# Optimization experiments

Hardware: AMD Instinct MI355X
Metric: run time of the kernel (lower is better)

## Reference

```python
import jax, jax.numpy as jnp
import numpy as np
import math

HIDDEN = 2048
NUM_HEADS = 16
NUM_KV_HEADS = 4
HEAD_DIM = HIDDEN // NUM_HEADS  # 128
INTER = 8192
ROPE_THETA = 10000.0
EPS = 1e-6
B, S = 1, 2048


def _linear_init(key, out_f, in_f):
    return jax.random.normal(key, (out_f, in_f), dtype=jnp.float32) * (2.0 / (in_f + out_f)) ** 0.5


def setup_inputs() -> dict:
    key = jax.random.key(0)
    ks = jax.random.split(key, 10)
    hidden_states = jax.random.normal(ks[0], (B, S, HIDDEN), dtype=jnp.float32)
    # additive causal mask [B, 1, S, S]
    causal = jnp.tril(jnp.ones((S, S), dtype=bool))
    attention_mask = jnp.where(causal, 0.0, -1e9).astype(jnp.float32)[None, None]
    position_ids = jnp.arange(S, dtype=jnp.int32)[None, :]
    return {
        "hidden_states": hidden_states,
        "attention_mask": attention_mask,
        "position_ids": position_ids,
        "norm1_w": jnp.ones((HIDDEN,), dtype=jnp.float32),
        "norm2_w": jnp.ones((HIDDEN,), dtype=jnp.float32),
        "Wq": _linear_init(ks[1], NUM_HEADS * HEAD_DIM, HIDDEN),
        "Wk": _linear_init(ks[2], NUM_KV_HEADS * HEAD_DIM, HIDDEN),
        "Wv": _linear_init(ks[3], NUM_KV_HEADS * HEAD_DIM, HIDDEN),
        "Wo": _linear_init(ks[4], HIDDEN, NUM_HEADS * HEAD_DIM),
        "Wgate": _linear_init(ks[5], INTER, HIDDEN),
        "Wup": _linear_init(ks[6], INTER, HIDDEN),
        "Wdown": _linear_init(ks[7], HIDDEN, INTER),
    }


def _rmsnorm(x, w):
    return x * jax.lax.rsqrt(jnp.mean(x * x, axis=-1, keepdims=True) + EPS) * w


def _apply_rope(x, position_ids):
    # x: [B, H, S, D]; split-half RoPE exactly as the torch module does
    half = x.shape[-1] // 2
    inv_freq = (1.0 / (ROPE_THETA ** (jnp.arange(0, HEAD_DIM, 2, dtype=jnp.float32) / HEAD_DIM)))[:half]
    freqs = jnp.einsum('bi,j->bij', position_ids.astype(jnp.float32), inv_freq)  # [B,S,half]
    cos = jnp.cos(freqs)[:, None]  # [B,1,S,half]
    sin = jnp.sin(freqs)[:, None]
    x1, x2 = x[..., :half], x[..., half:]
    return jnp.concatenate([x1 * cos - x2 * sin, x2 * cos + x1 * sin], axis=-1)


def reference(hidden_states, attention_mask, position_ids, norm1_w, norm2_w,
              Wq, Wk, Wv, Wo, Wgate, Wup, Wdown):
    b, s, _ = hidden_states.shape
    # --- attention sub-block (pre-norm residual) ---
    h = _rmsnorm(hidden_states, norm1_w)
    q = (h @ Wq.T).reshape(b, s, NUM_HEADS, HEAD_DIM).transpose(0, 2, 1, 3)
    k = (h @ Wk.T).reshape(b, s, NUM_KV_HEADS, HEAD_DIM).transpose(0, 2, 1, 3)
    v = (h @ Wv.T).reshape(b, s, NUM_KV_HEADS, HEAD_DIM).transpose(0, 2, 1, 3)
    q = _apply_rope(q, position_ids)
    k = _apply_rope(k, position_ids)
    n_rep = NUM_HEADS // NUM_KV_HEADS
    k = jnp.repeat(k, n_rep, axis=1)  # GQA repeat_interleave over head dim
    v = jnp.repeat(v, n_rep, axis=1)
    scores = jnp.einsum('bhqd,bhkd->bhqk', q, k) / math.sqrt(HEAD_DIM)
    scores = scores + attention_mask
    attn = jax.nn.softmax(scores, axis=-1)
    ctx = jnp.einsum('bhqk,bhkd->bhqd', attn, v).transpose(0, 2, 1, 3).reshape(b, s, -1)
    x = hidden_states + ctx @ Wo.T
    # --- MoE sub-block: num_experts == 1 -> plain SwiGLU MLP ---
    h2 = _rmsnorm(x, norm2_w)
    mlp = (jax.nn.silu(h2 @ Wgate.T) * (h2 @ Wup.T)) @ Wdown.T
    return x + mlp
```

## Files before the change

kernel.cpp:

```cpp
#include <hip/hip_runtime.h>
#include <hip/hip_bf16.h>
#include <math.h>


#define HIDDENC 2048
#define SLEN    2048
#define NHEADS  16
#define NKV     4
#define HD      128
#define INTERC  8192

typedef __attribute__((ext_vector_type(8))) short bf16x8;
typedef __attribute__((ext_vector_type(4))) float f32x4;
typedef __hip_bfloat16 bf16;

__device__ __forceinline__ void gld_lds16(const void* g, void* l) {
    __builtin_amdgcn_global_load_lds((const __attribute__((address_space(1))) void*)g,
                                     (__attribute__((address_space(3))) void*)l, 16, 0, 0);
}

__device__ __forceinline__ unsigned short bf_bits(float x) {
    bf16 t = __float2bfloat16(x);
    return *(unsigned short*)&t;
}
__device__ __forceinline__ float bits_f(short s) {
    bf16 b = *(bf16*)&s;
    return __bfloat162float(b);
}

#define SBAR      asm volatile("s_barrier" ::: "memory")
#define WAIT_VM4  asm volatile("s_waitcnt vmcnt(4)" ::: "memory")
#define WAIT_VM0  asm volatile("s_waitcnt vmcnt(0)" ::: "memory")

template <int EPI>
__global__ __launch_bounds__(256) void gemm_bt(const bf16* __restrict__ A,
                                               const bf16* __restrict__ B,
                                               void* __restrict__ Cout,
                                               const float* __restrict__ R,
                                               int M, int N, int K, int lda) {
    constexpr int BM = 128, BN = 128, BK = 64;
    __shared__ bf16 As[BM * BK];
    __shared__ bf16 Bs[BN * BK];
    const int tid  = threadIdx.x;
    const int wave = tid >> 6;
    const int lane = tid & 63;
    const int wm = wave >> 1, wn = wave & 1;
    const long m0 = (long)blockIdx.y * BM;
    const long n0 = (long)blockIdx.x * BN;

    const int srow = wave * 8 + (lane >> 3);
    const int scol = (lane & 7) * 8;
    const bf16* Ag = A + (m0 + srow) * (long)lda + scol;
    const bf16* Bg = B + (n0 + srow) * (long)lda + scol;
    bf16* Asw = &As[(wave * 8) * BK];
    bf16* Bsw = &Bs[(wave * 8) * BK];

    f32x4 acc[4][4] = {};
    const int row = lane & 15;
    const int kq  = (lane >> 4) * 8;

    for (int k0 = 0; k0 < K; k0 += BK) {
#pragma unroll
        for (int t = 0; t < 4; t++) {
            gld_lds16(Ag + (long)(t * 32) * lda + k0, Asw + t * 32 * BK);
            gld_lds16(Bg + (long)(t * 32) * lda + k0, Bsw + t * 32 * BK);
        }
        __syncthreads();
#pragma unroll
        for (int kk = 0; kk < BK; kk += 32) {
            bf16x8 af[4], bfr[4];
#pragma unroll
            for (int i = 0; i < 4; i++)
                af[i] = *(const bf16x8*)&As[(wm * 64 + i * 16 + row) * BK + kk + kq];
#pragma unroll
            for (int j = 0; j < 4; j++)
                bfr[j] = *(const bf16x8*)&Bs[(wn * 64 + j * 16 + row) * BK + kk + kq];
#pragma unroll
            for (int i = 0; i < 4; i++)
#pragma unroll
                for (int j = 0; j < 4; j++)
                    acc[i][j] = __builtin_amdgcn_mfma_f32_16x16x32_bf16(af[i], bfr[j], acc[i][j], 0, 0, 0);
        }
        __syncthreads();
    }

    const int quad = lane >> 4;
#pragma unroll
    for (int i = 0; i < 4; i++)
#pragma unroll
        for (int j = 0; j < 4; j++)
#pragma unroll
            for (int r = 0; r < 4; r++) {
                long rr = m0 + wm * 64 + i * 16 + quad * 4 + r;
                long cc = n0 + wn * 64 + j * 16 + (lane & 15);
                float v = acc[i][j][r];
                if (EPI == 0) {
                    ((bf16*)Cout)[rr * N + cc] = __float2bfloat16(v);
                } else {
                    ((float*)Cout)[rr * N + cc] = v + R[rr * N + cc];
                }
            }
}

template <int EPI>
__global__ __launch_bounds__(512) void gemm256(const bf16* __restrict__ A,
                                               const bf16* __restrict__ B,
                                               void* __restrict__ Cout,
                                               int M, int N, int K, int lda) {
    __shared__ __align__(16) bf16 smem[2][2][256 * 64];
    const int tid  = threadIdx.x;
    const int wave = tid >> 6, lane = tid & 63;
    const int wm = wave >> 2, wn = wave & 3;
    const int quad = lane >> 4, lrow = lane & 15;
    const long m0 = (long)blockIdx.y * 256;
    const long n0 = (long)blockIdx.x * 256;
    const long kofs = (long)blockIdx.z * K;

    const int srow  = tid >> 3;
    const int gphys = tid & 7;
    const int glog  = gphys ^ (srow & 7);
    const bf16* Ag = A + (m0 + srow) * (long)lda + kofs + glog * 8;
    const bf16* Bg = B + (n0 + srow) * (long)lda + kofs + glog * 8;

    auto stageA = [&](int tt) {
#pragma unroll
        for (int rr = 0; rr < 4; rr++)
            gld_lds16(Ag + ((long)tt << 6) + (long)(rr * 64) * lda,
                      &smem[tt & 1][0][tid * 8 + rr * 4096]);
    };
    auto stageB = [&](int tt, int hh) {
#pragma unroll
        for (int r2 = 0; r2 < 2; r2++) {
            int rr = hh * 2 + r2;
            gld_lds16(Bg + ((long)tt << 6) + (long)(rr * 64) * lda,
                      &smem[tt & 1][1][tid * 8 + rr * 4096]);
        }
    };

    f32x4 acc[8][4] = {};
    const int swz = (quad ^ (lrow & 7)) * 8;
    const int NT = K >> 6;

    stageA(0);
    stageB(0, 0); stageB(0, 1);
    if (NT > 1) { stageB(1, 0); stageB(1, 1); }
    WAIT_VM4;
    SBAR;

    for (int t = 0; t < NT; ++t) {
        const bf16* smA = &smem[t & 1][0][0];
        const bf16* smB = &smem[t & 1][1][0];
        bf16x8 bq[4][2], aq[2][2];

#pragma unroll
        for (int n = 0; n < 4; n++)
#pragma unroll
            for (int ks = 0; ks < 2; ks++)
                bq[n][ks] = *(const bf16x8*)&smB[(wn * 64 + n * 16 + lrow) * 64 + (swz ^ (ks * 32))];
#pragma unroll
        for (int i = 0; i < 2; i++)
#pragma unroll
            for (int ks = 0; ks < 2; ks++)
                aq[i][ks] = *(const bf16x8*)&smA[(wm * 128 + i * 16 + lrow) * 64 + (swz ^ (ks * 32))];
        if (t + 1 < NT) stageA(t + 1);
        SBAR;
        __builtin_amdgcn_s_setprio(1);
#pragma unroll
        for (int i = 0; i < 2; i++)
#pragma unroll
            for (int n = 0; n < 4; n++) {
                acc[i][n] = __builtin_amdgcn_mfma_f32_16x16x32_bf16(aq[i][0], bq[n][0], acc[i][n], 0, 0, 0);
                acc[i][n] = __builtin_amdgcn_mfma_f32_16x16x32_bf16(aq[i][1], bq[n][1], acc[i][n], 0, 0, 0);
            }
        __builtin_amdgcn_s_setprio(0);
        SBAR;

#pragma unroll
        for (int q = 1; q < 4; q++) {
#pragma unroll
            for (int i = 0; i < 2; i++)
#pragma unroll
                for (int ks = 0; ks < 2; ks++)
                    aq[i][ks] = *(const bf16x8*)&smA[(wm * 128 + (q * 2 + i) * 16 + lrow) * 64 + (swz ^ (ks * 32))];
            if (q == 1) { if (t + 2 < NT) stageB(t + 2, 0); }
            if (q == 2) { if (t + 2 < NT) stageB(t + 2, 1); }
            SBAR;
            __builtin_amdgcn_s_setprio(1);
#pragma unroll
            for (int i = 0; i < 2; i++)
#pragma unroll
                for (int n = 0; n < 4; n++) {
                    acc[q * 2 + i][n] = __builtin_amdgcn_mfma_f32_16x16x32_bf16(aq[i][0], bq[n][0], acc[q * 2 + i][n], 0, 0, 0);
                    acc[q * 2 + i][n] = __builtin_amdgcn_mfma_f32_16x16x32_bf16(aq[i][1], bq[n][1], acc[q * 2 + i][n], 0, 0, 0);
                }
            __builtin_amdgcn_s_setprio(0);
            if (q == 3) {
                if (t + 2 < NT) { WAIT_VM4; } else { WAIT_VM0; }
            }
            SBAR;
        }
    }

#pragma unroll
    for (int i = 0; i < 8; i++)
#pragma unroll
        for (int n = 0; n < 4; n++)
#pragma unroll
            for (int r = 0; r < 4; r++) {
                long rr = m0 + wm * 128 + i * 16 + quad * 4 + r;
                long cc = n0 + wn * 64 + n * 16 + lrow;
                float v = acc[i][n][r];
                if (EPI == 0) {
                    ((bf16*)Cout)[rr * N + cc] = __float2bfloat16(v);
                } else {
                    ((float*)Cout)[(long)blockIdx.z * M * N + rr * N + cc] = v;
                }
            }
}

__global__ __launch_bounds__(256) void rmsnorm_kernel(const float* __restrict__ x,
                                                      const float* __restrict__ w,
                                                      bf16* __restrict__ out) {
    const int row = blockIdx.x;
    const int tid = threadIdx.x;
    const float* xr = x + (long)row * HIDDENC;
    float4 a = *(const float4*)&xr[tid * 8];
    float4 b = *(const float4*)&xr[tid * 8 + 4];
    float ss = a.x*a.x + a.y*a.y + a.z*a.z + a.w*a.w + b.x*b.x + b.y*b.y + b.z*b.z + b.w*b.w;
#pragma unroll
    for (int d = 1; d < 64; d <<= 1) ss += __shfl_xor(ss, d, 64);
    __shared__ float wsum[4];
    if ((tid & 63) == 0) wsum[tid >> 6] = ss;
    __syncthreads();
    ss = wsum[0] + wsum[1] + wsum[2] + wsum[3];
    float sc = rsqrtf(ss * (1.0f / HIDDENC) + 1e-6f);
    float4 wa = *(const float4*)&w[tid * 8];
    float4 wb = *(const float4*)&w[tid * 8 + 4];
    float vals[8] = {a.x*wa.x, a.y*wa.y, a.z*wa.z, a.w*wa.w,
                     b.x*wb.x, b.y*wb.y, b.z*wb.z, b.w*wb.w};
    union { bf16x8 v; unsigned short u[8]; } pk;
#pragma unroll
    for (int e = 0; e < 8; e++) pk.u[e] = bf_bits(vals[e] * sc);
    *(bf16x8*)&out[(long)row * HIDDENC + tid * 8] = pk.v;
}

__global__ __launch_bounds__(256) void cvt_kernel(const float* __restrict__ in,
                                                  bf16* __restrict__ out, long n) {
    long idx = ((long)blockIdx.x * 256 + threadIdx.x) * 8;
    if (idx >= n) return;
    float4 a = *(const float4*)&in[idx];
    float4 b = *(const float4*)&in[idx + 4];
    float vals[8] = {a.x, a.y, a.z, a.w, b.x, b.y, b.z, b.w};
    union { bf16x8 v; unsigned short u[8]; } pk;
#pragma unroll
    for (int e = 0; e < 8; e++) pk.u[e] = bf_bits(vals[e]);
    *(bf16x8*)&out[idx] = pk.v;
}

__global__ __launch_bounds__(256) void rope_kernel(bf16* __restrict__ x,
                                                   const int* __restrict__ pos,
                                                   int nheads, int rowstride) {
    long gid = (long)blockIdx.x * 256 + threadIdx.x;
    int i = gid & 63;
    long t = gid >> 6;
    int h = (int)(t % nheads);
    long s = t / nheads;
    if (s >= SLEN) return;
    float inv = __expf(-(float)i * 0.14391156516779195f);
    float f = (float)pos[s] * inv;
    float sn, c;
    sincosf(f, &sn, &c);
    bf16* p = x + s * (long)rowstride + h * HD + i;
    float x1 = __bfloat162float(p[0]);
    float x2 = __bfloat162float(p[64]);
    p[0]  = __float2bfloat16(x1 * c - x2 * sn);
    p[64] = __float2bfloat16(x2 * c + x1 * sn);
}

__global__ __launch_bounds__(256) void flash_attn(const bf16* __restrict__ Q,
                                                  const bf16* __restrict__ Kb,
                                                  const bf16* __restrict__ VT,
                                                  bf16* __restrict__ Ctx) {
    constexpr int QSTR = 2560, PSTR = 68, BKEY = 64;
    __shared__ bf16 Ks[64 * 128];
    __shared__ bf16 Vs[128 * 64];
    __shared__ bf16 Ps[4][16 * PSTR];
    const int qt  = 31 - blockIdx.x;
    const int h   = blockIdx.y;
    const int kvh = h >> 2;
    const int tid = threadIdx.x;
    const int wave = tid >> 6, lane = tid & 63;
    const int quad = lane >> 4, lrow = lane & 15;
    const int qbase = qt * 64 + wave * 16;

    bf16x8 qf[4];
#pragma unroll
    for (int kk = 0; kk < 4; kk++)
        qf[kk] = *(const bf16x8*)&Q[(long)(qbase + lrow) * QSTR + h * HD + kk * 32 + quad * 8];

    f32x4 o[8] = {};
    float mrow[4], lsum[4];
#pragma unroll
    for (int r = 0; r < 4; r++) { mrow[r] = -1e30f; lsum[r] = 0.0f; }

    const int nkt = qt + 1;
    const float scale = 0.08838834764831845f;
    const bf16* Kh  = Kb + kvh * HD;
    const bf16* VTh = VT + (long)(kvh * HD) * SLEN;
    bf16* Pw = Ps[wave];

    for (int kt = 0; kt < nkt; kt++) {
        __syncthreads();
#pragma unroll
        for (int rd = 0; rd < 4; rd++) {
            int id = rd * 256 + tid;
            int row = id >> 4, g = id & 15;
            bf16x8 kv = *(const bf16x8*)&Kh[(long)(kt * BKEY + row) * QSTR + g * 8];
            *(bf16x8*)&Ks[row * 128 + ((g ^ (row & 15)) * 8)] = kv;
        }
#pragma unroll
        for (int rd = 0; rd < 4; rd++) {
            int id = rd * 256 + tid;
            int d = id >> 3, g = id & 7;
            bf16x8 vv = *(const bf16x8*)&VTh[(long)d * SLEN + kt * BKEY + g * 8];
            *(bf16x8*)&Vs[d * 64 + ((g ^ (d & 7)) * 8)] = vv;
        }
        __syncthreads();

        f32x4 sacc[4] = {};
#pragma unroll
        for (int kk = 0; kk < 4; kk++) {
            bf16x8 kb[4];
#pragma unroll
            for (int j = 0; j < 4; j++)
                kb[j] = *(const bf16x8*)&Ks[(j * 16 + lrow) * 128 + (((kk * 4 + quad) ^ lrow) * 8)];
#pragma unroll
            for (int j = 0; j < 4; j++)
                sacc[j] = __builtin_amdgcn_mfma_f32_16x16x32_bf16(qf[kk], kb[j], sacc[j], 0, 0, 0);
        }

        const bool diag = (kt == qt);
#pragma unroll
        for (int j = 0; j < 4; j++)
#pragma unroll
            for (int r = 0; r < 4; r++) {
                float v = sacc[j][r] * scale;
                if (diag) {
                    int rowg = qbase + quad * 4 + r;
                    int colg = qt * 64 + j * 16 + lrow;
                    if (colg > rowg) v = -1e30f;
                }
                sacc[j][r] = v;
            }

        float alpha[4];
#pragma unroll
        for (int r = 0; r < 4; r++) {
            float mx = sacc[0][r];
#pragma unroll
            for (int j = 1; j < 4; j++) mx = fmaxf(mx, sacc[j][r]);
#pragma unroll
            for (int d = 1; d < 16; d <<= 1) mx = fmaxf(mx, __shfl_xor(mx, d, 16));
            float mnew = fmaxf(mrow[r], mx);
            float a = __expf(mrow[r] - mnew);
            mrow[r] = mnew;
            alpha[r] = a;
            float rs = 0.0f;
#pragma unroll
            for (int j = 0; j < 4; j++) {
                float p = __expf(sacc[j][r] - mnew);
                sacc[j][r] = p;
                rs += p;
            }
#pragma unroll
            for (int d = 1; d < 16; d <<= 1) rs += __shfl_xor(rs, d, 16);
            lsum[r] = lsum[r] * a + rs;
        }

#pragma unroll
        for (int dj = 0; dj < 8; dj++)
#pragma unroll
            for (int r = 0; r < 4; r++) o[dj][r] *= alpha[r];

#pragma unroll
        for (int j = 0; j < 4; j++)
#pragma unroll
            for (int r = 0; r < 4; r++)
                Pw[(quad * 4 + r) * PSTR + j * 16 + lrow] = __float2bfloat16(sacc[j][r]);
        __asm__ volatile("s_waitcnt lgkmcnt(0)" ::: "memory");

#pragma unroll
        for (int kk = 0; kk < 2; kk++) {
            bf16x8 pf = *(const bf16x8*)&Pw[lrow * PSTR + kk * 32 + quad * 8];
#pragma unroll
            for (int dj = 0; dj < 8; dj++) {
                int dr = dj * 16 + lrow;
                bf16x8 vb = *(const bf16x8*)&Vs[dr * 64 + (((kk * 4 + quad) ^ (dr & 7)) * 8)];
                o[dj] = __builtin_amdgcn_mfma_f32_16x16x32_bf16(pf, vb, o[dj], 0, 0, 0);
            }
        }
    }

#pragma unroll
    for (int dj = 0; dj < 8; dj++)
#pragma unroll
        for (int r = 0; r < 4; r++) {
            long rowg = qbase + quad * 4 + r;
            long col  = (long)h * HD + dj * 16 + lrow;
            Ctx[rowg * (NHEADS * HD) + col] = __float2bfloat16(o[dj][r] / lsum[r]);
        }
}

__global__ __launch_bounds__(256) void silu_mul_kernel(const bf16* __restrict__ g,
                                                       const bf16* __restrict__ u,
                                                       bf16* __restrict__ out, long n) {
    long idx = ((long)blockIdx.x * 256 + threadIdx.x) * 8;
    if (idx >= n) return;
    bf16x8 gv = *(const bf16x8*)&g[idx];
    bf16x8 uv = *(const bf16x8*)&u[idx];
    union { bf16x8 v; unsigned short w[8]; } pk;
#pragma unroll
    for (int e = 0; e < 8; e++) {
        float gf = bits_f(gv[e]);
        float uf = bits_f(uv[e]);
        float s = gf / (1.0f + __expf(-gf));
        pk.w[e] = bf_bits(s * uf);
    }
    *(bf16x8*)&out[idx] = pk.v;
}

__global__ __launch_bounds__(256) void reduce4_kernel(const float* __restrict__ p,
                                                      float* __restrict__ out, long n) {
    long idx = ((long)blockIdx.x * 256 + threadIdx.x) * 4;
    if (idx >= n) return;
    float4 a = *(const float4*)&p[idx];
    float4 b = *(const float4*)&p[idx + n];
    float4 c = *(const float4*)&p[idx + 2 * n];
    float4 d = *(const float4*)&p[idx + 3 * n];
    float4 o = *(const float4*)&out[idx];
    o.x += a.x + b.x + c.x + d.x;
    o.y += a.y + b.y + c.y + d.y;
    o.z += a.z + b.z + c.z + d.z;
    o.w += a.w + b.w + c.w + d.w;
    *(float4*)&out[idx] = o;
}

extern "C" void kernel_launch(void* const* d_in, const int* in_sizes, int n_in,
                              void* d_out, int out_size, void* d_ws, size_t ws_size,
                              hipStream_t stream) {
    const float* hidden = (const float*)d_in[0];
    const int*   pos    = (const int*)d_in[2];
    const float* n1w    = (const float*)d_in[3];
    const float* n2w    = (const float*)d_in[4];
    const float* Wq     = (const float*)d_in[5];
    const float* Wk     = (const float*)d_in[6];
    const float* Wv     = (const float*)d_in[7];
    const float* Wo     = (const float*)d_in[8];
    const float* Wg     = (const float*)d_in[9];
    const float* Wu     = (const float*)d_in[10];
    const float* Wd     = (const float*)d_in[11];
    float* out = (float*)d_out;

    char* ws = (char*)d_ws;
    const size_t MB = 1ull << 20;
    bf16* h    = (bf16*)(ws + 0);
    bf16* qk   = (bf16*)(ws + 8  * MB);
    bf16* vt   = (bf16*)(ws + 18 * MB);
    bf16* ctx  = (bf16*)(ws + 20 * MB);
    bf16* wqk  = (bf16*)(ws + 28 * MB);
    bf16* wvb  = (bf16*)(ws + 38 * MB);
    bf16*  wg   = (bf16*)(ws + 8   * MB);
    bf16*  wu   = (bf16*)(ws + 40  * MB);
    bf16*  gate = (bf16*)(ws + 72  * MB);
    bf16*  up   = (bf16*)(ws + 104 * MB);
    bf16*  wd   = (bf16*)(ws + 104 * MB);
    float* pbuf = (float*)(ws + 0);
    bf16* wob = wqk;

    rmsnorm_kernel<<<dim3(2048), dim3(256), 0, stream>>>(hidden, n1w, h);
    cvt_kernel<<<dim3(2048), dim3(256), 0, stream>>>(Wq, wqk,                2048L * 2048);
    cvt_kernel<<<dim3(512),  dim3(256), 0, stream>>>(Wk, wqk + 2048L * 2048, 512L * 2048);
    cvt_kernel<<<dim3(512),  dim3(256), 0, stream>>>(Wv, wvb,                512L * 2048);
    gemm_bt<0><<<dim3(20, 16), dim3(256), 0, stream>>>(h, wqk, qk, nullptr, 2048, 2560, 2048, 2048);
    gemm_bt<0><<<dim3(16, 4),  dim3(256), 0, stream>>>(wvb, h, vt, nullptr, 512, 2048, 2048, 2048);
    rope_kernel<<<dim3(8192), dim3(256), 0, stream>>>(qk, pos, NHEADS, 2560);
    rope_kernel<<<dim3(2048), dim3(256), 0, stream>>>(qk + 2048, pos, NKV, 2560);
    flash_attn<<<dim3(32, 16), dim3(256), 0, stream>>>(qk, qk + 2048, vt, ctx);
    cvt_kernel<<<dim3(2048), dim3(256), 0, stream>>>(Wo, wob, 2048L * 2048);
    gemm_bt<1><<<dim3(16, 16), dim3(256), 0, stream>>>(ctx, wob, out, hidden, 2048, 2048, 2048, 2048);
    rmsnorm_kernel<<<dim3(2048), dim3(256), 0, stream>>>(out, n2w, h);
    cvt_kernel<<<dim3(8192), dim3(256), 0, stream>>>(Wg, wg, 8192L * 2048);
    cvt_kernel<<<dim3(8192), dim3(256), 0, stream>>>(Wu, wu, 8192L * 2048);
    gemm256<0><<<dim3(32, 8), dim3(512), 0, stream>>>(h, wg, gate, 2048, 8192, 2048, 2048);
    gemm256<0><<<dim3(32, 8), dim3(512), 0, stream>>>(h, wu, up,   2048, 8192, 2048, 2048);
    silu_mul_kernel<<<dim3(8192), dim3(256), 0, stream>>>(gate, up, gate, 2048L * 8192);
    cvt_kernel<<<dim3(8192), dim3(256), 0, stream>>>(Wd, wd, 2048L * 8192);
    gemm256<2><<<dim3(8, 8, 4), dim3(512), 0, stream>>>(gate, wd, pbuf, 2048, 2048, 2048, 8192);
    reduce4_kernel<<<dim3(4096), dim3(256), 0, stream>>>(pbuf, out, 2048L * 2048);
    (void)in_sizes; (void)n_in; (void)out_size; (void)ws_size;
}
```

Before: 758.3 us.

## Split attention KV range across two blocks with async LDS double-buffering; fuse SiLU-mul into up GEMM

Flash attention now launches two blocks per query tile, each handling alternating key tiles. Each block writes fp32 partial outputs plus row max and sum, and a new combine kernel merges the two halves. K/V loads use global_load_lds into double-buffered shared memory with priority hints around the MFMA sections, aiming to hide load latency and balance the causal workload. The SiLU-multiply is folded into the up-projection GEMM epilogue, which reads gate in place and removes the separate elementwise pass and the up buffer. The cost is extra fp32 traffic for the partials and one additional kernel launch.

```diff
diff --git a/kernel.cpp b/kernel.cpp
--- a/kernel.cpp
+++ b/kernel.cpp
@@ -106,6 +106,7 @@
 __global__ __launch_bounds__(512) void gemm256(const bf16* __restrict__ A,
                                                const bf16* __restrict__ B,
                                                void* __restrict__ Cout,
+                                               const bf16* __restrict__ Gg,
                                                int M, int N, int K, int lda) {
     __shared__ __align__(16) bf16 smem[2][2][256 * 64];
     const int tid  = threadIdx.x;
@@ -212,8 +213,12 @@
                 float v = acc[i][n][r];
                 if (EPI == 0) {
                     ((bf16*)Cout)[rr * N + cc] = __float2bfloat16(v);
+                } else if (EPI == 2) {
+                    ((float*)Cout)[(long)blockIdx.z * M * N + rr * N + cc] = v;
                 } else {
-                    ((float*)Cout)[(long)blockIdx.z * M * N + rr * N + cc] = v;
+                    float g = __bfloat162float(Gg[rr * N + cc]);
+                    float sg = g / (1.0f + __expf(-g));
+                    ((bf16*)Cout)[rr * N + cc] = __float2bfloat16(sg * v);
                 }
             }
 }
@@ -280,12 +285,14 @@
 __global__ __launch_bounds__(256) void flash_attn(const bf16* __restrict__ Q,
                                                   const bf16* __restrict__ Kb,
                                                   const bf16* __restrict__ VT,
-                                                  bf16* __restrict__ Ctx) {
+                                                  float* __restrict__ Opart,
+                                                  float* __restrict__ Ml) {
     constexpr int QSTR = 2560, PSTR = 68, BKEY = 64;
-    __shared__ bf16 Ks[64 * 128];
-    __shared__ bf16 Vs[128 * 64];
+    __shared__ bf16 Ks[2][64 * 128];
+    __shared__ bf16 Vs[2][128 * 64];
     __shared__ bf16 Ps[4][16 * PSTR];
-    const int qt  = 31 - blockIdx.x;
+    const int qt  = 31 - (int)(blockIdx.x >> 1);
+    const int sp  = blockIdx.x & 1;
     const int h   = blockIdx.y;
     const int kvh = h >> 2;
     const int tid = threadIdx.x;
@@ -303,41 +310,48 @@
 #pragma unroll
     for (int r = 0; r < 4; r++) { mrow[r] = -1e30f; lsum[r] = 0.0f; }
 
-    const int nkt = qt + 1;
     const float scale = 0.08838834764831845f;
     const bf16* Kh  = Kb + kvh * HD;
     const bf16* VTh = VT + (long)(kvh * HD) * SLEN;
     bf16* Pw = Ps[wave];
 
-    for (int kt = 0; kt < nkt; kt++) {
-        __syncthreads();
-#pragma unroll
-        for (int rd = 0; rd < 4; rd++) {
-            int id = rd * 256 + tid;
-            int row = id >> 4, g = id & 15;
-            bf16x8 kv = *(const bf16x8*)&Kh[(long)(kt * BKEY + row) * QSTR + g * 8];
-            *(bf16x8*)&Ks[row * 128 + ((g ^ (row & 15)) * 8)] = kv;
-        }
-#pragma unroll
-        for (int rd = 0; rd < 4; rd++) {
-            int id = rd * 256 + tid;
-            int d = id >> 3, g = id & 7;
-            bf16x8 vv = *(const bf16x8*)&VTh[(long)d * SLEN + kt * BKEY + g * 8];
-            *(bf16x8*)&Vs[d * 64 + ((g ^ (d & 7)) * 8)] = vv;
-        }
-        __syncthreads();
+    const int glogK = (tid & 15) ^ ((tid >> 4) & 15);
+    const int glogV = (tid & 7) ^ ((tid >> 3) & 7);
+    const bf16* KgB = Kh + (long)(tid >> 4) * QSTR + glogK * 8;
+    const bf16* VgB = VTh + (long)(tid >> 3) * SLEN + glogV * 8;
+
+    auto stage = [&](int kt, int b) {
+#pragma unroll
+        for (int rd = 0; rd < 4; rd++)
+            gld_lds16(KgB + (long)(kt * BKEY + rd * 16) * QSTR,
+                      &Ks[b][(rd * 256 + tid) * 8]);
+#pragma unroll
+        for (int rd = 0; rd < 4; rd++)
+            gld_lds16(VgB + (long)(rd * 32) * SLEN + kt * BKEY,
+                      &Vs[b][(rd * 256 + tid) * 8]);
+    };
+
+    int cur = 0;
+    stage(sp, 0);
+    WAIT_VM0;
+    __syncthreads();
+
+    for (int kt = sp; kt <= qt; kt += 2) {
+        if (kt + 2 <= qt) stage(kt + 2, cur ^ 1);
 
         f32x4 sacc[4] = {};
+        __builtin_amdgcn_s_setprio(1);
 #pragma unroll
         for (int kk = 0; kk < 4; kk++) {
             bf16x8 kb[4];
 #pragma unroll
             for (int j = 0; j < 4; j++)
-                kb[j] = *(const bf16x8*)&Ks[(j * 16 + lrow) * 128 + (((kk * 4 + quad) ^ lrow) * 8)];
+                kb[j] = *(const bf16x8*)&Ks[cur][(j * 16 + lrow) * 128 + (((kk * 4 + quad) ^ lrow) * 8)];
 #pragma unroll
             for (int j = 0; j < 4; j++)
                 sacc[j] = __builtin_amdgcn_mfma_f32_16x16x32_bf16(qf[kk], kb[j], sacc[j], 0, 0, 0);
         }
+        __builtin_amdgcn_s_setprio(0);
 
         const bool diag = (kt == qt);
 #pragma unroll
@@ -389,16 +403,21 @@
                 Pw[(quad * 4 + r) * PSTR + j * 16 + lrow] = __float2bfloat16(sacc[j][r]);
         __asm__ volatile("s_waitcnt lgkmcnt(0)" ::: "memory");
 
+        __builtin_amdgcn_s_setprio(1);
 #pragma unroll
         for (int kk = 0; kk < 2; kk++) {
             bf16x8 pf = *(const bf16x8*)&Pw[lrow * PSTR + kk * 32 + quad * 8];
 #pragma unroll
             for (int dj = 0; dj < 8; dj++) {
                 int dr = dj * 16 + lrow;
-                bf16x8 vb = *(const bf16x8*)&Vs[dr * 64 + (((kk * 4 + quad) ^ (dr & 7)) * 8)];
+                bf16x8 vb = *(const bf16x8*)&Vs[cur][dr * 64 + (((kk * 4 + quad) ^ (dr & 7)) * 8)];
                 o[dj] = __builtin_amdgcn_mfma_f32_16x16x32_bf16(pf, vb, o[dj], 0, 0, 0);
             }
         }
+        __builtin_amdgcn_s_setprio(0);
+
+        __syncthreads();
+        cur ^= 1;
     }
 
 #pragma unroll
@@ -407,26 +426,45 @@
         for (int r = 0; r < 4; r++) {
             long rowg = qbase + quad * 4 + r;
             long col  = (long)h * HD + dj * 16 + lrow;
-            Ctx[rowg * (NHEADS * HD) + col] = __float2bfloat16(o[dj][r] / lsum[r]);
-        }
-}
-
-__global__ __launch_bounds__(256) void silu_mul_kernel(const bf16* __restrict__ g,
-                                                       const bf16* __restrict__ u,
-                                                       bf16* __restrict__ out, long n) {
-    long idx = ((long)blockIdx.x * 256 + threadIdx.x) * 8;
-    if (idx >= n) return;
-    bf16x8 gv = *(const bf16x8*)&g[idx];
-    bf16x8 uv = *(const bf16x8*)&u[idx];
-    union { bf16x8 v; unsigned short w[8]; } pk;
-#pragma unroll
-    for (int e = 0; e < 8; e++) {
-        float gf = bits_f(gv[e]);
-        float uf = bits_f(uv[e]);
-        float s = gf / (1.0f + __expf(-gf));
-        pk.w[e] = bf_bits(s * uf);
+            Opart[(long)sp * SLEN * (NHEADS * HD) + rowg * (NHEADS * HD) + col] = o[dj][r];
+        }
+    if (lrow == 0) {
+#pragma unroll
+        for (int r = 0; r < 4; r++) {
+            long rowg = qbase + quad * 4 + r;
+            long mi = ((long)sp * SLEN + rowg) * (NHEADS * 2) + h * 2;
+            Ml[mi]     = mrow[r];
+            Ml[mi + 1] = lsum[r];
+        }
     }
-    *(bf16x8*)&out[idx] = pk.v;
+}
+
+__global__ __launch_bounds__(256) void attn_combine(const float* __restrict__ Opart,
+                                                    const float* __restrict__ Ml,
+                                                    bf16* __restrict__ Ctx) {
+    long gid = (long)blockIdx.x * 256 + threadIdx.x;
+    int oct = (int)(gid & 15);
+    long rh = gid >> 4;
+    int h = (int)(rh & 15);
+    long row = rh >> 4;
+    long mi0 = row * (NHEADS * 2) + h * 2;
+    long mi1 = ((long)SLEN + row) * (NHEADS * 2) + h * 2;
+    float m0 = Ml[mi0], l0 = Ml[mi0 + 1];
+    float m1 = Ml[mi1], l1 = Ml[mi1 + 1];
+    float m = fmaxf(m0, m1);
+    float w0 = __expf(m0 - m), w1 = __expf(m1 - m);
+    float inv = 1.0f / (w0 * l0 + w1 * l1);
+    long base = row * (NHEADS * HD) + h * HD + oct * 8;
+    float4 a0 = *(const float4*)&Opart[base];
+    float4 b0 = *(const float4*)&Opart[base + 4];
+    float4 a1 = *(const float4*)&Opart[(long)SLEN * (NHEADS * HD) + base];
+    float4 b1 = *(const float4*)&Opart[(long)SLEN * (NHEADS * HD) + base + 4];
+    float vals[8] = {w0*a0.x + w1*a1.x, w0*a0.y + w1*a1.y, w0*a0.z + w1*a1.z, w0*a0.w + w1*a1.w,
+                     w0*b0.x + w1*b1.x, w0*b0.y + w1*b1.y, w0*b0.z + w1*b1.z, w0*b0.w + w1*b1.w};
+    union { bf16x8 v; unsigned short u[8]; } pk;
+#pragma unroll
+    for (int e = 0; e < 8; e++) pk.u[e] = bf_bits(vals[e] * inv);
+    *(bf16x8*)&Ctx[base] = pk.v;
 }
 
 __global__ __launch_bounds__(256) void reduce4_kernel(const float* __restrict__ p,
@@ -469,10 +507,11 @@
     bf16* ctx  = (bf16*)(ws + 20 * MB);
     bf16* wqk  = (bf16*)(ws + 28 * MB);
     bf16* wvb  = (bf16*)(ws + 38 * MB);
+    float* opart = (float*)(ws + 40 * MB);
+    float* ml    = (float*)(ws + 72 * MB);
     bf16*  wg   = (bf16*)(ws + 8   * MB);
     bf16*  wu   = (bf16*)(ws + 40  * MB);
     bf16*  gate = (bf16*)(ws + 72  * MB);
-    bf16*  up   = (bf16*)(ws + 104 * MB);
     bf16*  wd   = (bf16*)(ws + 104 * MB);
     float* pbuf = (float*)(ws + 0);
     bf16* wob = wqk;
@@ -485,17 +524,17 @@
     gemm_bt<0><<<dim3(16, 4),  dim3(256), 0, stream>>>(wvb, h, vt, nullptr, 512, 2048, 2048, 2048);
     rope_kernel<<<dim3(8192), dim3(256), 0, stream>>>(qk, pos, NHEADS, 2560);
     rope_kernel<<<dim3(2048), dim3(256), 0, stream>>>(qk + 2048, pos, NKV, 2560);
-    flash_attn<<<dim3(32, 16), dim3(256), 0, stream>>>(qk, qk + 2048, vt, ctx);
+    flash_attn<<<dim3(64, 16), dim3(256), 0, stream>>>(qk, qk + 2048, vt, opart, ml);
+    attn_combine<<<dim3(2048), dim3(256), 0, stream>>>(opart, ml, ctx);
     cvt_kernel<<<dim3(2048), dim3(256), 0, stream>>>(Wo, wob, 2048L * 2048);
     gemm_bt<1><<<dim3(16, 16), dim3(256), 0, stream>>>(ctx, wob, out, hidden, 2048, 2048, 2048, 2048);
     rmsnorm_kernel<<<dim3(2048), dim3(256), 0, stream>>>(out, n2w, h);
     cvt_kernel<<<dim3(8192), dim3(256), 0, stream>>>(Wg, wg, 8192L * 2048);
     cvt_kernel<<<dim3(8192), dim3(256), 0, stream>>>(Wu, wu, 8192L * 2048);
-    gemm256<0><<<dim3(32, 8), dim3(512), 0, stream>>>(h, wg, gate, 2048, 8192, 2048, 2048);
-    gemm256<0><<<dim3(32, 8), dim3(512), 0, stream>>>(h, wu, up,   2048, 8192, 2048, 2048);
-    silu_mul_kernel<<<dim3(8192), dim3(256), 0, stream>>>(gate, up, gate, 2048L * 8192);
+    gemm256<0><<<dim3(32, 8), dim3(512), 0, stream>>>(h, wg, gate, nullptr, 2048, 8192, 2048, 2048);
+    gemm256<3><<<dim3(32, 8), dim3(512), 0, stream>>>(h, wu, gate, gate,    2048, 8192, 2048, 2048);
     cvt_kernel<<<dim3(8192), dim3(256), 0, stream>>>(Wd, wd, 2048L * 8192);
-    gemm256<2><<<dim3(8, 8, 4), dim3(512), 0, stream>>>(gate, wd, pbuf, 2048, 2048, 2048, 8192);
+    gemm256<2><<<dim3(8, 8, 4), dim3(512), 0, stream>>>(gate, wd, pbuf, nullptr, 2048, 2048, 2048, 8192);
     reduce4_kernel<<<dim3(4096), dim3(256), 0, stream>>>(pbuf, out, 2048L * 2048);
     (void)in_sizes; (void)n_in; (void)out_size; (void)ws_size;
 }
```

New measurement: 735.0 us. 1.03x faster.
